# Kernel optimization log

Hardware: AMD Instinct MI355X
Metric: run time of the kernel (lower is better)

## Reference

```python
import jax, jax.numpy as jnp
import numpy as np

NUM_NODES = 500_000
NUM_EDGES = 8_000_000
NUM_GRAPHS = 8_192


def gcn_conv(x, edge_index, W, b):
    """PyG GCNConv (default args): add self-loops, symmetric deg normalization.
    Messages flow source (row=edge_index[0]) -> target (col=edge_index[1])."""
    n = x.shape[0]
    loop = jnp.arange(n, dtype=edge_index.dtype)
    row = jnp.concatenate([edge_index[0], loop])
    col = jnp.concatenate([edge_index[1], loop])
    h = x @ W  # [n, out]
    deg = jax.ops.segment_sum(jnp.ones_like(col, dtype=x.dtype), col, num_segments=n)
    dinv = jnp.where(deg > 0, jax.lax.rsqrt(deg), 0.0)
    norm = dinv[row] * dinv[col]  # [E+n]
    msg = h[row] * norm[:, None]  # gather + scale
    out = jax.ops.segment_sum(msg, col, num_segments=n)  # scatter-add at targets
    return out + b


def global_mean_pool(x, batch, num_graphs):
    s = jax.ops.segment_sum(x, batch, num_segments=num_graphs)
    cnt = jax.ops.segment_sum(jnp.ones((x.shape[0],), dtype=x.dtype), batch, num_segments=num_graphs)
    return s / jnp.maximum(cnt, 1.0)[:, None]


def setup_inputs() -> dict:
    key = jax.random.key(0)
    ks = jax.random.split(key, 12)
    x = jax.random.normal(ks[0], (NUM_NODES, 9), dtype=jnp.float32)
    edge_index = jax.random.randint(ks[1], (2, NUM_EDGES), 0, NUM_NODES, dtype=jnp.int64)
    batch = jnp.sort(jax.random.randint(ks[2], (NUM_NODES,), 0, NUM_GRAPHS, dtype=jnp.int64))
    metadata = jax.random.normal(ks[3], (NUM_GRAPHS, 27), dtype=jnp.float32)
    def glorot(k, shape):
        lim = float(np.sqrt(6.0 / (shape[0] + shape[1])))
        return jax.random.uniform(k, shape, jnp.float32, -lim, lim)
    W1 = glorot(ks[4], (9, 16));  b1 = jnp.zeros((16,), jnp.float32)
    W2 = glorot(ks[5], (16, 16)); b2 = jnp.zeros((16,), jnp.float32)
    Wh1 = glorot(ks[6], (16 + 27, 16)); bh1 = jnp.zeros((16,), jnp.float32)
    Wh2 = glorot(ks[7], (16, 1));       bh2 = jnp.zeros((1,), jnp.float32)
    return {"x": x, "edge_index": edge_index, "batch": batch, "metadata": metadata,
            "W1": W1, "b1": b1, "W2": W2, "b2": b2,
            "Wh1": Wh1, "bh1": bh1, "Wh2": Wh2, "bh2": bh2}


def reference(x, edge_index, batch, metadata, W1, b1, W2, b2, Wh1, bh1, Wh2, bh2):
    # eval mode: dropout is identity
    h = jax.nn.relu(gcn_conv(x, edge_index, W1, b1))
    h = jax.nn.relu(gcn_conv(h, edge_index, W2, b2))
    emb = global_mean_pool(h, batch, metadata.shape[0])  # [G, 16]
    z = jnp.concatenate([emb, metadata], axis=1)          # [G, 43]
    z = jax.nn.relu(z @ Wh1 + bh1)
    return z @ Wh2 + bh2  # [G, 1]
```

## Files before the change

### kernel.cpp

```cpp
#include <hip/hip_runtime.h>

#define N_NODES 500000
#define N_EDGES 8000000
#define N_GRAPHS 8192
#define BKT 512
#define NBK 977
#define C_CAP 9216
#define TILE2 8192
#define NTB2 977
#define CSR_IT 9

__device__ __forceinline__ void bf2x(unsigned u, float& lo, float& hi) {
    union { unsigned i; float f; } a, b;
    a.i = u << 16; b.i = u & 0xFFFF0000u;
    lo = a.f; hi = b.f;
}
__device__ __forceinline__ unsigned f2bf2(float lo, float hi) {
    union { float f; unsigned i; } a, b;
    a.f = lo; b.f = hi;
    unsigned rl = (a.i + 0x7FFFu + ((a.i >> 16) & 1u)) >> 16;
    unsigned rh = (b.i + 0x7FFFu + ((b.i >> 16) & 1u)) & 0xFFFF0000u;
    return rl | rh;
}
__device__ __forceinline__ void addbf(float* acc, uint4 a) {
    float lo, hi;
    bf2x(a.x, lo, hi); acc[0] += lo; acc[1] += hi;
    bf2x(a.y, lo, hi); acc[2] += lo; acc[3] += hi;
    bf2x(a.z, lo, hi); acc[4] += lo; acc[5] += hi;
    bf2x(a.w, lo, hi); acc[6] += lo; acc[7] += hi;
}

__global__ void k_init(float* __restrict__ pooled, int* __restrict__ gcursor) {
    int i = blockIdx.x * 256 + threadIdx.x;
    if (i < N_GRAPHS * 17) pooled[i] = 0.0f;
    if (i < NBK) gcursor[i] = i * C_CAP;
}

__global__ __launch_bounds__(1024) void
k_build(const int4* __restrict__ row4, const int4* __restrict__ col4,
        int* __restrict__ gcursor, unsigned* __restrict__ packed, int E) {
    __shared__ unsigned sortedv[TILE2];
    __shared__ unsigned short sortedb[TILE2];
    __shared__ int hist2[2][1024];
    __shared__ int lbase[1024];
    __shared__ int runbase[1024];
    __shared__ int sd[1024];
    int t = threadIdx.x, b = blockIdx.x;
    int sub = t >> 9;
    hist2[0][t] = 0; hist2[1][t] = 0;
    __syncthreads();
    unsigned uval[8];
    unsigned short ub[8];
#pragma unroll
    for (int k = 0; k < 2; k++) {
        int vi = b * 2048 + k * 1024 + t;
        int j0 = k * 4;
        if (vi * 4 < E) {
            int4 c = col4[vi];
            int4 r = row4[vi];
            unsigned cc, rr;
            cc = (unsigned)c.x; rr = (unsigned)r.x;
            if (cc < N_NODES && rr < N_NODES) { uval[j0] = (rr << 9) | (cc & 511u); ub[j0] = (unsigned short)(cc >> 9); atomicAdd(&hist2[sub][cc >> 9], 1); } else ub[j0] = 0xFFFFu;
            cc = (unsigned)c.y; rr = (unsigned)r.y;
            if (cc < N_NODES && rr < N_NODES) { uval[j0+1] = (rr << 9) | (cc & 511u); ub[j0+1] = (unsigned short)(cc >> 9); atomicAdd(&hist2[sub][cc >> 9], 1); } else ub[j0+1] = 0xFFFFu;
            cc = (unsigned)c.z; rr = (unsigned)r.z;
            if (cc < N_NODES && rr < N_NODES) { uval[j0+2] = (rr << 9) | (cc & 511u); ub[j0+2] = (unsigned short)(cc >> 9); atomicAdd(&hist2[sub][cc >> 9], 1); } else ub[j0+2] = 0xFFFFu;
            cc = (unsigned)c.w; rr = (unsigned)r.w;
            if (cc < N_NODES && rr < N_NODES) { uval[j0+3] = (rr << 9) | (cc & 511u); ub[j0+3] = (unsigned short)(cc >> 9); atomicAdd(&hist2[sub][cc >> 9], 1); } else ub[j0+3] = 0xFFFFu;
        } else {
            ub[j0] = 0xFFFFu; ub[j0+1] = 0xFFFFu; ub[j0+2] = 0xFFFFu; ub[j0+3] = 0xFFFFu;
        }
    }
    __syncthreads();
    int tot = (t < NBK) ? (hist2[0][t] + hist2[1][t]) : 0;
    sd[t] = tot; __syncthreads();
    for (int d = 1; d < 1024; d <<= 1) {
        int tv = (t >= d) ? sd[t - d] : 0;
        __syncthreads(); sd[t] += tv; __syncthreads();
    }
    lbase[t] = sd[t] - tot;
    if (t < NBK && tot) runbase[t] = atomicAdd(&gcursor[t], tot);
    hist2[0][t] = 0;
    __syncthreads();
    int total = sd[1023];
#pragma unroll
    for (int j = 0; j < 8; j++) {
        unsigned bb = ub[j];
        if (bb != 0xFFFFu) {
            int l = lbase[bb] + atomicAdd(&hist2[0][bb], 1);
            sortedv[l] = uval[j];
            sortedb[l] = (unsigned short)bb;
        }
    }
    __syncthreads();
    for (int l = t; l < total; l += 1024) {
        int bb = sortedb[l];
        packed[runbase[bb] + (l - lbase[bb])] = sortedv[l];
    }
}

__global__ __launch_bounds__(1024) void
k_csr(const unsigned* __restrict__ packed, const int* __restrict__ gcursor,
      int* __restrict__ srcs, int* __restrict__ rowptr,
      float* __restrict__ dinv_g, int N) {
    __shared__ int sortedv[C_CAP];
    __shared__ int hist2[2][BKT];
    __shared__ int off[BKT];
    __shared__ int sd[1024];
    __shared__ int sgbase;
    int t = threadIdx.x, b = blockIdx.x;
    int h = t >> 9;
    sd[t] = (t < b) ? (gcursor[t] - t * C_CAP) : 0;
    __syncthreads();
    for (int d = 512; d > 0; d >>= 1) {
        if (t < d) sd[t] += sd[t + d];
        __syncthreads();
    }
    if (t == 0) sgbase = sd[0];
    ((int*)hist2)[t] = 0;
    __syncthreads();
    int gbase = sgbase;
    int cnt = gcursor[b] - b * C_CAP;
    int sfix = b * C_CAP;
    unsigned pw[CSR_IT];
#pragma unroll
    for (int k = 0; k < CSR_IT; k++) {
        int i = k * 1024 + t;
        if (i < cnt) {
            unsigned w = packed[sfix + i];
            pw[k] = w;
            atomicAdd(&hist2[h][w & 511u], 1);
        } else pw[k] = 0xFFFFFFFFu;
    }
    __syncthreads();
    int ls = (t < BKT) ? (hist2[0][t] + hist2[1][t]) : 0;
    sd[t] = ls; __syncthreads();
    for (int d = 1; d < BKT; d <<= 1) {
        int tv = (t >= d) ? sd[t - d] : 0;
        __syncthreads(); sd[t] += tv; __syncthreads();
    }
    if (t < BKT) {
        int myoff = sd[t] - ls;
        off[t] = myoff;
        int v = b * BKT + t;
        if (v < N) {
            rowptr[v] = gbase + myoff;
            dinv_g[v] = rsqrtf(1.0f + (float)ls);
        }
    }
    if (b == NBK - 1 && t == 0) rowptr[N] = gbase + cnt;
    __syncthreads();
    if (t < BKT) hist2[0][t] = 0;
    __syncthreads();
#pragma unroll
    for (int k = 0; k < CSR_IT; k++) {
        unsigned w = pw[k];
        if (w != 0xFFFFFFFFu) {
            unsigned c = w & 511u;
            int l = off[c] + atomicAdd(&hist2[0][c], 1);
            sortedv[l] = (int)(w >> 9);
        }
    }
    __syncthreads();
    for (int l = t; l < cnt; l += 1024) srcs[gbase + l] = sortedv[l];
}

__global__ void k_l1(const float* __restrict__ x, const float* __restrict__ W1,
                     const float* __restrict__ dinv, uint4* __restrict__ hsu, int n) {
    int v = blockIdx.x * 256 + threadIdx.x;
    if (v >= n) return;
    float xi[9];
#pragma unroll
    for (int k = 0; k < 9; k++) xi[k] = x[v * 9 + k];
    float di = dinv[v];
    float h[16];
#pragma unroll
    for (int j = 0; j < 16; j++) {
        float acc = 0.f;
#pragma unroll
        for (int k = 0; k < 9; k++) acc += xi[k] * W1[k * 16 + j];
        h[j] = acc * di;
    }
    uint4 w0, w1;
    w0.x = f2bf2(h[0], h[1]);  w0.y = f2bf2(h[2], h[3]);
    w0.z = f2bf2(h[4], h[5]);  w0.w = f2bf2(h[6], h[7]);
    w1.x = f2bf2(h[8], h[9]);  w1.y = f2bf2(h[10], h[11]);
    w1.z = f2bf2(h[12], h[13]); w1.w = f2bf2(h[14], h[15]);
    hsu[v * 2] = w0;
    hsu[v * 2 + 1] = w1;
}

__global__ void k_pullA(const int* __restrict__ rowptr, const int* __restrict__ srcs,
                        const uint4* __restrict__ hsu, const float* __restrict__ dinv,
                        const float* __restrict__ b1, const float* __restrict__ W2,
                        uint4* __restrict__ hs2u, int N) {
    int tid = blockIdx.x * 256 + threadIdx.x;
    int v = tid >> 1;
    int q = tid & 1;
    if (v >= N) return;
    int s = rowptr[v], e = rowptr[v + 1];
    float acc[8];
    {
        uint4 u = hsu[v * 2 + q];
        bf2x(u.x, acc[0], acc[1]); bf2x(u.y, acc[2], acc[3]);
        bf2x(u.z, acc[4], acc[5]); bf2x(u.w, acc[6], acc[7]);
    }
    int k = s;
    for (; k + 8 <= e; k += 8) {
        int r0 = __builtin_nontemporal_load(&srcs[k]);
        int r1 = __builtin_nontemporal_load(&srcs[k + 1]);
        int r2 = __builtin_nontemporal_load(&srcs[k + 2]);
        int r3 = __builtin_nontemporal_load(&srcs[k + 3]);
        int r4 = __builtin_nontemporal_load(&srcs[k + 4]);
        int r5 = __builtin_nontemporal_load(&srcs[k + 5]);
        int r6 = __builtin_nontemporal_load(&srcs[k + 6]);
        int r7 = __builtin_nontemporal_load(&srcs[k + 7]);
        uint4 a0 = hsu[r0 * 2 + q];
        uint4 a1 = hsu[r1 * 2 + q];
        uint4 a2 = hsu[r2 * 2 + q];
        uint4 a3 = hsu[r3 * 2 + q];
        uint4 a4 = hsu[r4 * 2 + q];
        uint4 a5 = hsu[r5 * 2 + q];
        uint4 a6 = hsu[r6 * 2 + q];
        uint4 a7 = hsu[r7 * 2 + q];
        addbf(acc, a0); addbf(acc, a1); addbf(acc, a2); addbf(acc, a3);
        addbf(acc, a4); addbf(acc, a5); addbf(acc, a6); addbf(acc, a7);
    }
    for (; k + 4 <= e; k += 4) {
        int r0 = __builtin_nontemporal_load(&srcs[k]);
        int r1 = __builtin_nontemporal_load(&srcs[k + 1]);
        int r2 = __builtin_nontemporal_load(&srcs[k + 2]);
        int r3 = __builtin_nontemporal_load(&srcs[k + 3]);
        uint4 a0 = hsu[r0 * 2 + q];
        uint4 a1 = hsu[r1 * 2 + q];
        uint4 a2 = hsu[r2 * 2 + q];
        uint4 a3 = hsu[r3 * 2 + q];
        addbf(acc, a0); addbf(acc, a1); addbf(acc, a2); addbf(acc, a3);
    }
    for (; k < e; k++) addbf(acc, hsu[__builtin_nontemporal_load(&srcs[k]) * 2 + q]);
    float di = dinv[v];
    float h1[8];
#pragma unroll
    for (int i = 0; i < 8; i++) {
        float tt = acc[i] * di + b1[q * 8 + i];
        h1[i] = tt > 0.f ? tt : 0.f;
    }
    float o[8] = {0.f, 0.f, 0.f, 0.f, 0.f, 0.f, 0.f, 0.f};
#pragma unroll
    for (int kk = 0; kk < 16; kk++) {
        float hk = __shfl(h1[kk & 7], kk >> 3, 2);
#pragma unroll
        for (int i = 0; i < 8; i++) o[i] += hk * W2[kk * 16 + q * 8 + i];
    }
#pragma unroll
    for (int i = 0; i < 8; i++) o[i] *= di;
    uint4 w;
    w.x = f2bf2(o[0], o[1]); w.y = f2bf2(o[2], o[3]);
    w.z = f2bf2(o[4], o[5]); w.w = f2bf2(o[6], o[7]);
    hs2u[v * 2 + q] = w;
}

__global__ void k_pullB(const int* __restrict__ rowptr, const int* __restrict__ srcs,
                        const uint4* __restrict__ hs2u, const float* __restrict__ dinv,
                        const float* __restrict__ b2, const int* __restrict__ batch,
                        float* __restrict__ pooled, float* __restrict__ cnt, int N) {
    int tid = blockIdx.x * 256 + threadIdx.x;
    int v = tid >> 1;
    int q = tid & 1;
    if (v >= N) return;
    int s = rowptr[v], e = rowptr[v + 1];
    float acc[8];
    {
        uint4 u = hs2u[v * 2 + q];
        bf2x(u.x, acc[0], acc[1]); bf2x(u.y, acc[2], acc[3]);
        bf2x(u.z, acc[4], acc[5]); bf2x(u.w, acc[6], acc[7]);
    }
    int k = s;
    for (; k + 8 <= e; k += 8) {
        int r0 = __builtin_nontemporal_load(&srcs[k]);
        int r1 = __builtin_nontemporal_load(&srcs[k + 1]);
        int r2 = __builtin_nontemporal_load(&srcs[k + 2]);
        int r3 = __builtin_nontemporal_load(&srcs[k + 3]);
        int r4 = __builtin_nontemporal_load(&srcs[k + 4]);
        int r5 = __builtin_nontemporal_load(&srcs[k + 5]);
        int r6 = __builtin_nontemporal_load(&srcs[k + 6]);
        int r7 = __builtin_nontemporal_load(&srcs[k + 7]);
        uint4 a0 = hs2u[r0 * 2 + q];
        uint4 a1 = hs2u[r1 * 2 + q];
        uint4 a2 = hs2u[r2 * 2 + q];
        uint4 a3 = hs2u[r3 * 2 + q];
        uint4 a4 = hs2u[r4 * 2 + q];
        uint4 a5 = hs2u[r5 * 2 + q];
        uint4 a6 = hs2u[r6 * 2 + q];
        uint4 a7 = hs2u[r7 * 2 + q];
        addbf(acc, a0); addbf(acc, a1); addbf(acc, a2); addbf(acc, a3);
        addbf(acc, a4); addbf(acc, a5); addbf(acc, a6); addbf(acc, a7);
    }
    for (; k + 4 <= e; k += 4) {
        int r0 = __builtin_nontemporal_load(&srcs[k]);
        int r1 = __builtin_nontemporal_load(&srcs[k + 1]);
        int r2 = __builtin_nontemporal_load(&srcs[k + 2]);
        int r3 = __builtin_nontemporal_load(&srcs[k + 3]);
        uint4 a0 = hs2u[r0 * 2 + q];
        uint4 a1 = hs2u[r1 * 2 + q];
        uint4 a2 = hs2u[r2 * 2 + q];
        uint4 a3 = hs2u[r3 * 2 + q];
        addbf(acc, a0); addbf(acc, a1); addbf(acc, a2); addbf(acc, a3);
    }
    for (; k < e; k++) addbf(acc, hs2u[__builtin_nontemporal_load(&srcs[k]) * 2 + q]);
    float di = dinv[v];
    float h2[8];
#pragma unroll
    for (int i = 0; i < 8; i++) {
        float tt = acc[i] * di + b2[q * 8 + i];
        h2[i] = tt > 0.f ? tt : 0.f;
    }
    int l = threadIdx.x & 63;
    int g = batch[v];
    float c = (q == 0) ? 1.0f : 0.0f;
#pragma unroll
    for (int off = 2; off <= 32; off <<= 1) {
        int pg = __shfl_up(g, off, 64);
        float pc = __shfl_up(c, off, 64);
        float p0 = __shfl_up(h2[0], off, 64);
        float p1 = __shfl_up(h2[1], off, 64);
        float p2 = __shfl_up(h2[2], off, 64);
        float p3 = __shfl_up(h2[3], off, 64);
        float p4 = __shfl_up(h2[4], off, 64);
        float p5 = __shfl_up(h2[5], off, 64);
        float p6 = __shfl_up(h2[6], off, 64);
        float p7 = __shfl_up(h2[7], off, 64);
        if (l >= off && pg == g) {
            c += pc;
            h2[0] += p0; h2[1] += p1; h2[2] += p2; h2[3] += p3;
            h2[4] += p4; h2[5] += p5; h2[6] += p6; h2[7] += p7;
        }
    }
    int gn = __shfl_down(g, 2, 64);
    bool tail = (l >= 62) || (gn != g);
    if (tail) {
#pragma unroll
        for (int i = 0; i < 8; i++)
            atomicAdd(&pooled[g * 16 + q * 8 + i], h2[i]);
        if (q == 0) atomicAdd(&cnt[g], c);
    }
}

__global__ void k_head(const float* __restrict__ pooled, const float* __restrict__ cnt,
                       const float* __restrict__ meta, const float* __restrict__ Wh1,
                       const float* __restrict__ bh1, const float* __restrict__ Wh2,
                       const float* __restrict__ bh2, float* __restrict__ out, int G) {
    int g = blockIdx.x * 256 + threadIdx.x;
    if (g >= G) return;
    float z[43];
    float c = cnt[g];
    c = c > 1.f ? c : 1.f;
#pragma unroll
    for (int j = 0; j < 16; j++) z[j] = pooled[g * 16 + j] / c;
#pragma unroll
    for (int j = 0; j < 27; j++) z[16 + j] = meta[g * 27 + j];
    float acc2 = bh2[0];
#pragma unroll
    for (int jj = 0; jj < 16; jj++) {
        float a = bh1[jj];
#pragma unroll
        for (int k = 0; k < 43; k++) a += z[k] * Wh1[k * 16 + jj];
        a = a > 0.f ? a : 0.f;
        acc2 += a * Wh2[jj];
    }
    out[g] = acc2;
}

extern "C" void kernel_launch(void* const* d_in, const int* in_sizes, int n_in,
                              void* d_out, int out_size, void* d_ws, size_t ws_size,
                              hipStream_t stream) {
    const float* x    = (const float*)d_in[0];
    const int*   ei   = (const int*)d_in[1];
    const int*   batch= (const int*)d_in[2];
    const float* meta = (const float*)d_in[3];
    const float* W1   = (const float*)d_in[4];
    const float* b1   = (const float*)d_in[5];
    const float* W2   = (const float*)d_in[6];
    const float* b2   = (const float*)d_in[7];
    const float* Wh1  = (const float*)d_in[8];
    const float* bh1  = (const float*)d_in[9];
    const float* Wh2  = (const float*)d_in[10];
    const float* bh2  = (const float*)d_in[11];
    float* out = (float*)d_out;

    const int N = N_NODES, E = N_EDGES, G = N_GRAPHS;
    const int* row = ei;
    const int* col = ei + E;

    float*    ws      = (float*)d_ws;
    float*    dinv    = ws;
    unsigned* packed  = (unsigned*)(ws + 512000);
    int*      srcs    = (int*)(packed + 9004032);
    float*    pooled  = (float*)(srcs + 8000000);
    float*    cnt     = pooled + G * 16;
    int*      gcursor = (int*)(cnt + G);
    int*      rowptr  = gcursor + 1024;
    unsigned* hsu     = packed;
    unsigned* hs2u    = packed + 4000000;

    dim3 blk(256);
    int gN = (N + 255) / 256;

    k_init<<<(G * 17 + 255) / 256, blk, 0, stream>>>(pooled, gcursor);
    k_build<<<NTB2, dim3(1024), 0, stream>>>((const int4*)row, (const int4*)col,
                                             gcursor, packed, E);
    k_csr<<<NBK, dim3(1024), 0, stream>>>(packed, gcursor, srcs, rowptr, dinv, N);

    k_l1<<<gN, blk, 0, stream>>>(x, W1, dinv, (uint4*)hsu, N);
    int gP2 = (N * 2 + 255) / 256;
    k_pullA<<<gP2, blk, 0, stream>>>(rowptr, srcs, (const uint4*)hsu, dinv,
                                     b1, W2, (uint4*)hs2u, N);

    k_pullB<<<gP2, blk, 0, stream>>>(rowptr, srcs, (const uint4*)hs2u, dinv,
                                     b2, batch, pooled, cnt, N);

    k_head<<<(G + 255) / 256, blk, 0, stream>>>(pooled, cnt, meta, Wh1, bh1, Wh2, bh2, out, G);
}
```

Measured before the change: 456.1 us.

## Store layer-1 features as FP8, fuse X·W1 into CSR kernel, one thread per node

The layer-1 transformed features are now packed as 16 FP8 e4m3 values (16 bytes per node) instead of 32 bytes of bf16. The X·W1 projection is moved into the CSR build kernel, which removes the separate k_l1 launch and a reread of dinv. k_pullA now uses one thread per node gathering a single uint4, halving gather traffic and removing the lane-pair shuffle. hsu and hs2u move to their own workspace regions. FP8 storage adds quantization error to the first aggregation, and the per-thread work in pullA grows (16 accumulators, a 16x16 matvec, no 8-wide unroll), which may reduce memory-level parallelism.

Measured after the change: 425.4 us. 1.07x faster.

```diff
diff --git a/kernel.cpp b/kernel.cpp
--- a/kernel.cpp
+++ b/kernel.cpp
@@ -1,4 +1,5 @@
 #include <hip/hip_runtime.h>
+#include <hip/hip_fp8.h>
 
 #define N_NODES 500000
 #define N_EDGES 8000000
@@ -9,6 +10,49 @@
 #define TILE2 8192
 #define NTB2 977
 #define CSR_IT 9
+
+typedef __attribute__((ext_vector_type(2))) float v2f;
+
+#if __has_builtin(__builtin_amdgcn_cvt_pk_f32_fp8)
+template <bool HI>
+__device__ __forceinline__ v2f cvt2fp8(unsigned w) {
+    return __builtin_amdgcn_cvt_pk_f32_fp8((int)w, HI);
+}
+#else
+template <bool HI>
+__device__ __forceinline__ v2f cvt2fp8(unsigned w) {
+    unsigned h16 = HI ? (w >> 16) : (w & 0xFFFFu);
+    __hip_fp8_e4m3 a, b;
+    a.__x = (__hip_fp8_storage_t)(h16 & 0xFFu);
+    b.__x = (__hip_fp8_storage_t)(h16 >> 8);
+    v2f r; r.x = (float)a; r.y = (float)b; return r;
+}
+#endif
+#if __has_builtin(__builtin_amdgcn_cvt_pk_fp8_f32)
+__device__ __forceinline__ unsigned pk4fp8(float a, float b, float c, float d) {
+    int r = 0;
+    r = __builtin_amdgcn_cvt_pk_fp8_f32(a, b, r, false);
+    r = __builtin_amdgcn_cvt_pk_fp8_f32(c, d, r, true);
+    return (unsigned)r;
+}
+#else
+__device__ __forceinline__ unsigned pk4fp8(float a, float b, float c, float d) {
+    __hip_fp8_e4m3 qa(a), qb(b), qc(c), qd(d);
+    return (unsigned)qa.__x | ((unsigned)qb.__x << 8) |
+           ((unsigned)qc.__x << 16) | ((unsigned)qd.__x << 24);
+}
+#endif
+__device__ __forceinline__ void addfp8x16(float* acc, uint4 a) {
+    v2f p;
+    p = cvt2fp8<false>(a.x); acc[0] += p.x; acc[1] += p.y;
+    p = cvt2fp8<true>(a.x);  acc[2] += p.x; acc[3] += p.y;
+    p = cvt2fp8<false>(a.y); acc[4] += p.x; acc[5] += p.y;
+    p = cvt2fp8<true>(a.y);  acc[6] += p.x; acc[7] += p.y;
+    p = cvt2fp8<false>(a.z); acc[8] += p.x; acc[9] += p.y;
+    p = cvt2fp8<true>(a.z);  acc[10] += p.x; acc[11] += p.y;
+    p = cvt2fp8<false>(a.w); acc[12] += p.x; acc[13] += p.y;
+    p = cvt2fp8<true>(a.w);  acc[14] += p.x; acc[15] += p.y;
+}
 
 __device__ __forceinline__ void bf2x(unsigned u, float& lo, float& hi) {
     union { unsigned i; float f; } a, b;
@@ -101,16 +145,19 @@
 
 __global__ __launch_bounds__(1024) void
 k_csr(const unsigned* __restrict__ packed, const int* __restrict__ gcursor,
+      const float* __restrict__ x, const float* __restrict__ W1,
       int* __restrict__ srcs, int* __restrict__ rowptr,
-      float* __restrict__ dinv_g, int N) {
+      float* __restrict__ dinv_g, uint4* __restrict__ hsu, int N) {
     __shared__ int sortedv[C_CAP];
     __shared__ int hist2[2][BKT];
     __shared__ int off[BKT];
     __shared__ int sd[1024];
     __shared__ int sgbase;
+    __shared__ float sW1[144];
     int t = threadIdx.x, b = blockIdx.x;
     int h = t >> 9;
     sd[t] = (t < b) ? (gcursor[t] - t * C_CAP) : 0;
+    if (t < 144) sW1[t] = W1[t];
     __syncthreads();
     for (int d = 512; d > 0; d >>= 1) {
         if (t < d) sd[t] += sd[t + d];
@@ -139,13 +186,14 @@
         int tv = (t >= d) ? sd[t - d] : 0;
         __syncthreads(); sd[t] += tv; __syncthreads();
     }
+    int v = b * BKT + t;
+    float di = rsqrtf(1.0f + (float)ls);
     if (t < BKT) {
         int myoff = sd[t] - ls;
         off[t] = myoff;
-        int v = b * BKT + t;
         if (v < N) {
             rowptr[v] = gbase + myoff;
-            dinv_g[v] = rsqrtf(1.0f + (float)ls);
+            dinv_g[v] = di;
         }
     }
     if (b == NBK - 1 && t == 0) rowptr[N] = gbase + cnt;
@@ -163,101 +211,77 @@
     }
     __syncthreads();
     for (int l = t; l < cnt; l += 1024) srcs[gbase + l] = sortedv[l];
-}
-
-__global__ void k_l1(const float* __restrict__ x, const float* __restrict__ W1,
-                     const float* __restrict__ dinv, uint4* __restrict__ hsu, int n) {
-    int v = blockIdx.x * 256 + threadIdx.x;
-    if (v >= n) return;
-    float xi[9];
-#pragma unroll
-    for (int k = 0; k < 9; k++) xi[k] = x[v * 9 + k];
-    float di = dinv[v];
-    float h[16];
-#pragma unroll
-    for (int j = 0; j < 16; j++) {
-        float acc = 0.f;
-#pragma unroll
-        for (int k = 0; k < 9; k++) acc += xi[k] * W1[k * 16 + j];
-        h[j] = acc * di;
-    }
-    uint4 w0, w1;
-    w0.x = f2bf2(h[0], h[1]);  w0.y = f2bf2(h[2], h[3]);
-    w0.z = f2bf2(h[4], h[5]);  w0.w = f2bf2(h[6], h[7]);
-    w1.x = f2bf2(h[8], h[9]);  w1.y = f2bf2(h[10], h[11]);
-    w1.z = f2bf2(h[12], h[13]); w1.w = f2bf2(h[14], h[15]);
-    hsu[v * 2] = w0;
-    hsu[v * 2 + 1] = w1;
+    if (t < BKT && v < N) {
+        float xi[9];
+#pragma unroll
+        for (int k = 0; k < 9; k++) xi[k] = x[v * 9 + k];
+        float hh[16];
+#pragma unroll
+        for (int j = 0; j < 16; j++) {
+            float acc = 0.f;
+#pragma unroll
+            for (int k = 0; k < 9; k++) acc += xi[k] * sW1[k * 16 + j];
+            hh[j] = acc * di;
+        }
+        uint4 w;
+        w.x = pk4fp8(hh[0], hh[1], hh[2], hh[3]);
+        w.y = pk4fp8(hh[4], hh[5], hh[6], hh[7]);
+        w.z = pk4fp8(hh[8], hh[9], hh[10], hh[11]);
+        w.w = pk4fp8(hh[12], hh[13], hh[14], hh[15]);
+        hsu[v] = w;
+    }
 }
 
 __global__ void k_pullA(const int* __restrict__ rowptr, const int* __restrict__ srcs,
                         const uint4* __restrict__ hsu, const float* __restrict__ dinv,
                         const float* __restrict__ b1, const float* __restrict__ W2,
                         uint4* __restrict__ hs2u, int N) {
-    int tid = blockIdx.x * 256 + threadIdx.x;
-    int v = tid >> 1;
-    int q = tid & 1;
+    int v = blockIdx.x * 256 + threadIdx.x;
     if (v >= N) return;
     int s = rowptr[v], e = rowptr[v + 1];
-    float acc[8];
+    float acc[16];
     {
-        uint4 u = hsu[v * 2 + q];
-        bf2x(u.x, acc[0], acc[1]); bf2x(u.y, acc[2], acc[3]);
-        bf2x(u.z, acc[4], acc[5]); bf2x(u.w, acc[6], acc[7]);
+        uint4 u = hsu[v];
+#pragma unroll
+        for (int i = 0; i < 16; i++) acc[i] = 0.f;
+        addfp8x16(acc, u);
     }
     int k = s;
-    for (; k + 8 <= e; k += 8) {
-        int r0 = __builtin_nontemporal_load(&srcs[k]);
-        int r1 = __builtin_nontemporal_load(&srcs[k + 1]);
-        int r2 = __builtin_nontemporal_load(&srcs[k + 2]);
-        int r3 = __builtin_nontemporal_load(&srcs[k + 3]);
-        int r4 = __builtin_nontemporal_load(&srcs[k + 4]);
-        int r5 = __builtin_nontemporal_load(&srcs[k + 5]);
-        int r6 = __builtin_nontemporal_load(&srcs[k + 6]);
-        int r7 = __builtin_nontemporal_load(&srcs[k + 7]);
-        uint4 a0 = hsu[r0 * 2 + q];
-        uint4 a1 = hsu[r1 * 2 + q];
-        uint4 a2 = hsu[r2 * 2 + q];
-        uint4 a3 = hsu[r3 * 2 + q];
-        uint4 a4 = hsu[r4 * 2 + q];
-        uint4 a5 = hsu[r5 * 2 + q];
-        uint4 a6 = hsu[r6 * 2 + q];
-        uint4 a7 = hsu[r7 * 2 + q];
-        addbf(acc, a0); addbf(acc, a1); addbf(acc, a2); addbf(acc, a3);
-        addbf(acc, a4); addbf(acc, a5); addbf(acc, a6); addbf(acc, a7);
-    }
     for (; k + 4 <= e; k += 4) {
         int r0 = __builtin_nontemporal_load(&srcs[k]);
         int r1 = __builtin_nontemporal_load(&srcs[k + 1]);
         int r2 = __builtin_nontemporal_load(&srcs[k + 2]);
         int r3 = __builtin_nontemporal_load(&srcs[k + 3]);
-        uint4 a0 = hsu[r0 * 2 + q];
-        uint4 a1 = hsu[r1 * 2 + q];
-        uint4 a2 = hsu[r2 * 2 + q];
-        uint4 a3 = hsu[r3 * 2 + q];
-        addbf(acc, a0); addbf(acc, a1); addbf(acc, a2); addbf(acc, a3);
-    }
-    for (; k < e; k++) addbf(acc, hsu[__builtin_nontemporal_load(&srcs[k]) * 2 + q]);
+        uint4 a0 = hsu[r0];
+        uint4 a1 = hsu[r1];
+        uint4 a2 = hsu[r2];
+        uint4 a3 = hsu[r3];
+        addfp8x16(acc, a0); addfp8x16(acc, a1);
+        addfp8x16(acc, a2); addfp8x16(acc, a3);
+    }
+    for (; k < e; k++) addfp8x16(acc, hsu[__builtin_nontemporal_load(&srcs[k])]);
     float di = dinv[v];
-    float h1[8];
-#pragma unroll
-    for (int i = 0; i < 8; i++) {
-        float tt = acc[i] * di + b1[q * 8 + i];
+    float h1[16];
+#pragma unroll
+    for (int i = 0; i < 16; i++) {
+        float tt = acc[i] * di + b1[i];
         h1[i] = tt > 0.f ? tt : 0.f;
     }
-    float o[8] = {0.f, 0.f, 0.f, 0.f, 0.f, 0.f, 0.f, 0.f};
+    float o[16];
+#pragma unroll
+    for (int i = 0; i < 16; i++) o[i] = 0.f;
 #pragma unroll
     for (int kk = 0; kk < 16; kk++) {
-        float hk = __shfl(h1[kk & 7], kk >> 3, 2);
-#pragma unroll
-        for (int i = 0; i < 8; i++) o[i] += hk * W2[kk * 16 + q * 8 + i];
-    }
-#pragma unroll
-    for (int i = 0; i < 8; i++) o[i] *= di;
-    uint4 w;
-    w.x = f2bf2(o[0], o[1]); w.y = f2bf2(o[2], o[3]);
-    w.z = f2bf2(o[4], o[5]); w.w = f2bf2(o[6], o[7]);
-    hs2u[v * 2 + q] = w;
+#pragma unroll
+        for (int i = 0; i < 16; i++) o[i] += h1[kk] * W2[kk * 16 + i];
+    }
+    uint4 w0, w1;
+    w0.x = f2bf2(o[0] * di, o[1] * di);  w0.y = f2bf2(o[2] * di, o[3] * di);
+    w0.z = f2bf2(o[4] * di, o[5] * di);  w0.w = f2bf2(o[6] * di, o[7] * di);
+    w1.x = f2bf2(o[8] * di, o[9] * di);  w1.y = f2bf2(o[10] * di, o[11] * di);
+    w1.z = f2bf2(o[12] * di, o[13] * di); w1.w = f2bf2(o[14] * di, o[15] * di);
+    hs2u[v * 2] = w0;
+    hs2u[v * 2 + 1] = w1;
 }
 
 __global__ void k_pullB(const int* __restrict__ rowptr, const int* __restrict__ srcs,
@@ -396,26 +420,25 @@
     float*    dinv    = ws;
     unsigned* packed  = (unsigned*)(ws + 512000);
     int*      srcs    = (int*)(packed + 9004032);
-    float*    pooled  = (float*)(srcs + 8000000);
+    unsigned* hsu     = (unsigned*)(srcs + 8000000);
+    unsigned* hs2u    = hsu + 2000000;
+    float*    pooled  = (float*)(hs2u + 4000000);
     float*    cnt     = pooled + G * 16;
     int*      gcursor = (int*)(cnt + G);
     int*      rowptr  = gcursor + 1024;
-    unsigned* hsu     = packed;
-    unsigned* hs2u    = packed + 4000000;
 
     dim3 blk(256);
-    int gN = (N + 255) / 256;
 
     k_init<<<(G * 17 + 255) / 256, blk, 0, stream>>>(pooled, gcursor);
     k_build<<<NTB2, dim3(1024), 0, stream>>>((const int4*)row, (const int4*)col,
                                              gcursor, packed, E);
-    k_csr<<<NBK, dim3(1024), 0, stream>>>(packed, gcursor, srcs, rowptr, dinv, N);
-
-    k_l1<<<gN, blk, 0, stream>>>(x, W1, dinv, (uint4*)hsu, N);
+    k_csr<<<NBK, dim3(1024), 0, stream>>>(packed, gcursor, x, W1,
+                                          srcs, rowptr, dinv, (uint4*)hsu, N);
+
+    k_pullA<<<(N + 255) / 256, blk, 0, stream>>>(rowptr, srcs, (const uint4*)hsu,
+                                                 dinv, b1, W2, (uint4*)hs2u, N);
+
     int gP2 = (N * 2 + 255) / 256;
-    k_pullA<<<gP2, blk, 0, stream>>>(rowptr, srcs, (const uint4*)hsu, dinv,
-                                     b1, W2, (uint4*)hs2u, N);
-
     k_pullB<<<gP2, blk, 0, stream>>>(rowptr, srcs, (const uint4*)hs2u, dinv,
                                      b2, batch, pooled, cnt, N);
 
```
